# Performance work log

Measured on AMD Instinct MI355X. Metric: run time of the kernel, lower is better.

The kernel has to match this reference:

```python
import jax, jax.numpy as jnp
import numpy as np

NUM_HEADS = 16
HEAD_DIM = 64
D_MODEL = 1024
WINDOW = 256
ROPE_BASE = 10000.0
LN_EPS = 1e-5


def setup_inputs() -> dict:
    key = jax.random.key(0)
    k1, k2, k3, k4 = jax.random.split(key, 4)
    B, S, D = 1, 2048, D_MODEL
    x = jax.random.normal(k1, (B, S, D), dtype=jnp.float32)
    state = jax.random.normal(k2, (B, D), dtype=jnp.float32)
    # nn.Linear(d, 3d, bias=False): y = x @ W_qkv with W_qkv: [D, 3D]
    W_qkv = jax.random.normal(k3, (D, 3 * D), dtype=jnp.float32) / np.sqrt(D)
    W_out = jax.random.normal(k4, (D, D), dtype=jnp.float32) / np.sqrt(D)
    ln_gamma = jnp.ones((D,), dtype=jnp.float32)
    ln_beta = jnp.zeros((D,), dtype=jnp.float32)
    return {"x": x, "state": state, "W_qkv": W_qkv, "W_out": W_out,
            "ln_gamma": ln_gamma, "ln_beta": ln_beta}


def _rotate_half(t):
    h = t.shape[-1] // 2
    return jnp.concatenate([-t[..., h:], t[..., :h]], axis=-1)


def _rope(q, k):
    # q, k: [B, H, S, Hd]
    S, Hd = q.shape[2], q.shape[3]
    inv_freq = 1.0 / (ROPE_BASE ** (jnp.arange(0, Hd, 2, dtype=jnp.float32) / Hd))
    ang = jnp.arange(S, dtype=jnp.float32)[:, None] * inv_freq[None, :]  # [S, Hd/2]
    cos = jnp.concatenate([jnp.cos(ang), jnp.cos(ang)], axis=-1)[None, None]  # [1,1,S,Hd]
    sin = jnp.concatenate([jnp.sin(ang), jnp.sin(ang)], axis=-1)[None, None]
    return q * cos + _rotate_half(q) * sin, k * cos + _rotate_half(k) * sin


def _local_causal_mask(S):
    idx = jnp.arange(S)
    dist = idx[:, None] - idx[None, :]
    allowed = (dist >= 0) & (dist <= WINDOW)
    # Faithful to source: allowed positions get 1.0 (softmax-shift-invariant), else -inf
    return jnp.where(allowed, 1.0, -jnp.inf).astype(jnp.float32)[None, None]


def reference(x, state, W_qkv, W_out, ln_gamma, ln_beta):
    B, S, D = x.shape
    H, Hd = NUM_HEADS, HEAD_DIM
    qkv = (x @ W_qkv).reshape(B, S, 3, H, Hd).transpose(2, 0, 3, 1, 4)  # [3,B,H,S,Hd]
    q, k, v = qkv[0], qkv[1], qkv[2]
    q, k = _rope(q, k)
    scores = jnp.einsum("bhsd,bhtd->bhst", q, k) / np.sqrt(Hd) + _local_causal_mask(S)
    attn = jax.nn.softmax(scores, axis=-1)
    out = jnp.einsum("bhst,bhtd->bhsd", attn, v)  # [B,H,S,Hd]
    out = out.transpose(0, 2, 1, 3).reshape(B, S, D)
    res = x + out @ W_out
    mu = jnp.mean(res, axis=-1, keepdims=True)
    var = jnp.var(res, axis=-1, keepdims=True)
    y = (res - mu) * jax.lax.rsqrt(var + LN_EPS) * ln_gamma + ln_beta
    return y, state
```

## Files before the change

### kernel.cpp

```cpp
#include <hip/hip_runtime.h>
#include <math.h>

#define S_LEN 2048
#define DMODEL 1024
#define NHEADS 16
#define HDIM 64
#define WIN 256
#define N_QKV 3072

typedef __attribute__((ext_vector_type(8))) short s16x8;
typedef __attribute__((ext_vector_type(8))) _Float16 f16x8;
typedef __attribute__((ext_vector_type(4))) _Float16 f16x4;
typedef __attribute__((ext_vector_type(4))) float f32x4;

typedef __attribute__((address_space(1))) const void gas_void;
typedef __attribute__((address_space(3))) void las_void;

__device__ inline unsigned short f2bf(float f) {
    unsigned int u = __float_as_uint(f);
    u += 0x7FFFu + ((u >> 16) & 1u);
    return (unsigned short)(u >> 16);
}
__device__ inline float bf2f(unsigned short h) {
    return __uint_as_float(((unsigned int)h) << 16);
}

__global__ __launch_bounds__(256) void cvt_f16(
    const float* __restrict__ src, _Float16* __restrict__ dst)
{
    int i = blockIdx.x * 256 + threadIdx.x;
    float4 v = *(const float4*)&src[i * 4];
    f16x4 o;
    o[0] = (_Float16)v.x; o[1] = (_Float16)v.y;
    o[2] = (_Float16)v.z; o[3] = (_Float16)v.w;
    *(f16x4*)&dst[i * 4] = o;
}

__global__ __launch_bounds__(256) void rope_tab_k(float2* __restrict__ tab)
{
    int idx = blockIdx.x * 256 + threadIdx.x;
    int s = idx >> 5, i = idx & 31;
    float inv = expf(-(float)i * 0.2878231366242553f);
    float ang = (float)s * inv;
    tab[idx] = make_float2(cosf(ang), sinf(ang));
}

__global__ __launch_bounds__(256) void transpose_cvt(
    const float* __restrict__ W, _Float16* __restrict__ T, int K, int N)
{
    __shared__ float t[32][33];
    const int tx = threadIdx.x & 31;
    const int ty = threadIdx.x >> 5;
    const int n0 = blockIdx.x * 32, k0 = blockIdx.y * 32;

    #pragma unroll
    for (int i = 0; i < 4; ++i)
        t[ty + i * 8][tx] = W[(size_t)(k0 + ty + i * 8) * N + n0 + tx];
    __syncthreads();
    #pragma unroll
    for (int i = 0; i < 4; ++i) {
        int n = n0 + ty + i * 8;
        T[(size_t)n * K + k0 + tx] = (_Float16)t[tx][ty + i * 8];
    }
}

template<int BM, int BN, bool RES>
__global__ __launch_bounds__(256) void gemm_lds(
    const _Float16* __restrict__ A, const _Float16* __restrict__ B,
    const float* __restrict__ resid, float* __restrict__ C,
    int M, int N, int K)
{
    constexpr int WM = BM / 2, WN = BN / 2;
    constexpr int MI = WM / 16, NJ = WN / 16;

    __shared__ _Float16 As[BM * 32];
    __shared__ _Float16 Bs[BN * 32];

    const int tid = threadIdx.x;
    const int w = tid >> 6, lane = tid & 63;
    const int m16 = lane & 15, g = lane >> 4;
    const int wr = w >> 1, wc = w & 1;
    const int bm = blockIdx.y * BM, bn = blockIdx.x * BN;

    const int srow = lane >> 2;
    const int sgran = (lane & 3) ^ (srow & 3);

    f32x4 acc[MI][NJ];
    #pragma unroll
    for (int i = 0; i < MI; ++i)
        #pragma unroll
        for (int j = 0; j < NJ; ++j) acc[i][j] = (f32x4)(0.0f);

    for (int kt = 0; kt < K / 32; ++kt) {
        const int k0 = kt * 32;
        __syncthreads();
        #pragma unroll
        for (int p = 0; p < BM / 64; ++p) {
            int row = p * 64 + w * 16 + srow;
            __builtin_amdgcn_global_load_lds(
                (gas_void*)&A[(size_t)(bm + row) * K + k0 + sgran * 8],
                (las_void*)&As[(p * 64 + w * 16) * 32], 16, 0, 0);
        }
        #pragma unroll
        for (int p = 0; p < BN / 64; ++p) {
            int row = p * 64 + w * 16 + srow;
            __builtin_amdgcn_global_load_lds(
                (gas_void*)&B[(size_t)(bn + row) * K + k0 + sgran * 8],
                (las_void*)&Bs[(p * 64 + w * 16) * 32], 16, 0, 0);
        }
        __syncthreads();

        f16x8 af[MI], bf_[NJ];
        #pragma unroll
        for (int i = 0; i < MI; ++i) {
            int row = wr * WM + i * 16 + m16;
            af[i] = *(const f16x8*)&As[row * 32 + ((g ^ (row & 3)) << 3)];
        }
        #pragma unroll
        for (int j = 0; j < NJ; ++j) {
            int row = wc * WN + j * 16 + m16;
            bf_[j] = *(const f16x8*)&Bs[row * 32 + ((g ^ (row & 3)) << 3)];
        }
        #pragma unroll
        for (int j = 0; j < NJ; ++j)
            #pragma unroll
            for (int i = 0; i < MI; ++i)
                acc[i][j] = __builtin_amdgcn_mfma_f32_16x16x32_f16(
                    af[i], bf_[j], acc[i][j], 0, 0, 0);
    }

    const int g4 = g * 4;
    #pragma unroll
    for (int i = 0; i < MI; ++i)
        #pragma unroll
        for (int j = 0; j < NJ; ++j) {
            int col = bn + wc * WN + j * 16 + m16;
            #pragma unroll
            for (int r = 0; r < 4; ++r) {
                int row = bm + wr * WM + i * 16 + g4 + r;
                float val = acc[i][j][r];
                if (RES) val += resid[(size_t)row * N + col];
                C[(size_t)row * N + col] = val;
            }
        }
}

__global__ __launch_bounds__(256) void rope_scatter(
    const float* __restrict__ qkv, const float2* __restrict__ tab,
    _Float16* __restrict__ qf, _Float16* __restrict__ kf)
{
    int idx = blockIdx.x * 256 + threadIdx.x;
    int s  = idx >> 10;
    int r  = idx & 1023;
    int hd = r & 63;
    int h  = r >> 6;
    const float* row = qkv + (size_t)s * N_QKV;

    float qv = row[r];
    float kv = row[DMODEL + r];

    float2 cs = tab[s * 32 + (hd & 31)];
    int   pr  = (hd < 32) ? r + 32 : r - 32;
    float sgn = (hd < 32) ? -1.0f : 1.0f;

    float qo = (qv * cs.x + sgn * row[pr] * cs.y) * 0.125f;
    float ko =  kv * cs.x + sgn * row[DMODEL + pr] * cs.y;

    size_t o = ((size_t)h * S_LEN + s) * HDIM + hd;
    qf[o] = (_Float16)qo;
    kf[o] = (_Float16)ko;
}

__global__ __launch_bounds__(256) void v_transpose(
    const float* __restrict__ qkv, unsigned short* __restrict__ vT)
{
    __shared__ float t[64][65];
    const int s0 = blockIdx.x * 64;
    const int h  = blockIdx.y;
    const int tid = threadIdx.x;
    const int dq  = (tid & 15) * 4;
    const int sl0 = tid >> 4;

    #pragma unroll
    for (int p = 0; p < 4; ++p) {
        int sl = sl0 + p * 16;
        float4 v = *(const float4*)&qkv[(size_t)(s0 + sl) * N_QKV + 2 * DMODEL + h * HDIM + dq];
        t[sl][dq] = v.x; t[sl][dq + 1] = v.y; t[sl][dq + 2] = v.z; t[sl][dq + 3] = v.w;
    }
    __syncthreads();
    #pragma unroll
    for (int p = 0; p < 2; ++p) {
        int u = tid + p * 256;
        int d = u >> 3, sb = (u & 7) * 8;
        s16x8 o;
        #pragma unroll
        for (int i = 0; i < 8; ++i) o[i] = (short)f2bf(t[sb + i][d]);
        *(s16x8*)&vT[((size_t)h * HDIM + d) * S_LEN + s0 + sb] = o;
    }
}

#define KP 72
__global__ __launch_bounds__(256, 3) void attn_mfma(
    const _Float16* __restrict__ qg, const _Float16* __restrict__ kg,
    const unsigned short* __restrict__ vTg, _Float16* __restrict__ oh)
{
    __shared__ __align__(16) _Float16 Ks[64][KP];
    __shared__ __align__(16) unsigned short Vt[64][KP];
    __shared__ __align__(16) unsigned short Pw[4][16][40];

    const int h   = blockIdx.y;
    const int s0  = blockIdx.x * 64;
    const int tid = threadIdx.x;
    const int w   = tid >> 6, lane = tid & 63;
    const int m16 = lane & 15, g = lane >> 4;
    const int t_base = s0 - 256;

    const int qrow = s0 + w * 16 + m16;
    const _Float16* qp = qg + ((size_t)h * S_LEN + qrow) * HDIM;
    f16x8 qf[2];
    qf[0] = *(const f16x8*)&qp[g * 8];
    qf[1] = *(const f16x8*)&qp[32 + g * 8];

    const int qb_ = w * 16 + m16;
    int lo_b = 256 - s0; if (lo_b < qb_) lo_b = qb_;
    const int hi_b = qb_ + 256;

    f32x4 O[4];
    #pragma unroll
    for (int nt = 0; nt < 4; ++nt) O[nt] = (f32x4)(0.0f);
    float l_r[4] = {0.0f, 0.0f, 0.0f, 0.0f};
    float m_col = -1e30f;

    const int stage_min = (s0 >= 256) ? 0 : ((193 - s0 + 63) >> 6);

    for (int st = stage_min; st < 5; ++st) {
        __syncthreads();
        const int t0s = t_base + st * 64;
        #pragma unroll
        for (int pp = 0; pp < 2; ++pp) {
            int u = tid + pp * 256;
            int row = u >> 3, cb = (u & 7) * 8;
            int t = t0s + row;
            f16x8 kv = {};
            if (t >= 0)
                kv = *(const f16x8*)&kg[((size_t)h * S_LEN + t) * HDIM + cb];
            *(f16x8*)&Ks[row][cb] = kv;
        }
        #pragma unroll
        for (int pp = 0; pp < 2; ++pp) {
            int u = tid + pp * 256;
            int d = u >> 3, kb = (u & 7) * 8;
            int t = t0s + kb;
            s16x8 vv = {};
            if (t >= 0)
                vv = *(const s16x8*)&vTg[((size_t)h * HDIM + d) * S_LEN + t];
            *(s16x8*)&Vt[d][kb] = vv;
        }
        __syncthreads();

        #pragma unroll
        for (int ch = 0; ch < 2; ++ch) {
            f32x4 sc[2];
            #pragma unroll
            for (int kt2 = 0; kt2 < 2; ++kt2) {
                int krow = ch * 32 + kt2 * 16 + m16;
                f16x8 k0 = *(const f16x8*)&Ks[krow][g * 8];
                f16x8 k1 = *(const f16x8*)&Ks[krow][32 + g * 8];
                f32x4 a = (f32x4)(0.0f);
                a = __builtin_amdgcn_mfma_f32_16x16x32_f16(k0, qf[0], a, 0, 0, 0);
                a = __builtin_amdgcn_mfma_f32_16x16x32_f16(k1, qf[1], a, 0, 0, 0);
                sc[kt2] = a;
            }

            float scm[8];
            float pmax = -1e30f;
            #pragma unroll
            for (int kt2 = 0; kt2 < 2; ++kt2)
                #pragma unroll
                for (int r = 0; r < 4; ++r) {
                    int ki = st * 64 + ch * 32 + kt2 * 16 + 4 * g + r;
                    bool vd = (ki >= lo_b) && (ki <= hi_b);
                    float s_ = vd ? sc[kt2][r] : -1e30f;
                    scm[kt2 * 4 + r] = s_;
                    pmax = fmaxf(pmax, s_);
                }
            pmax = fmaxf(pmax, __shfl_xor(pmax, 16));
            pmax = fmaxf(pmax, __shfl_xor(pmax, 32));
            float mnew = fmaxf(m_col, pmax);

            float p[8];
            float psum = 0.0f;
            #pragma unroll
            for (int i = 0; i < 8; ++i) {
                float e = (scm[i] > -9e29f) ? __expf(scm[i] - mnew) : 0.0f;
                p[i] = e;
                psum += e;
            }
            psum += __shfl_xor(psum, 16);
            psum += __shfl_xor(psum, 32);
            float scale = __expf(m_col - mnew);
            m_col = mnew;

            #pragma unroll
            for (int r = 0; r < 4; ++r) {
                float sr = __shfl(scale, 4 * g + r);
                float ps = __shfl(psum, 4 * g + r);
                l_r[r] = l_r[r] * sr + ps;
                O[0][r] *= sr; O[1][r] *= sr; O[2][r] *= sr; O[3][r] *= sr;
            }

            unsigned int d0, d1, d2, d3;
            asm("v_cvt_pk_bf16_f32 %0, %1, %2" : "=v"(d0) : "v"(p[0]), "v"(p[1]));
            asm("v_cvt_pk_bf16_f32 %0, %1, %2" : "=v"(d1) : "v"(p[2]), "v"(p[3]));
            asm("v_cvt_pk_bf16_f32 %0, %1, %2" : "=v"(d2) : "v"(p[4]), "v"(p[5]));
            asm("v_cvt_pk_bf16_f32 %0, %1, %2" : "=v"(d3) : "v"(p[6]), "v"(p[7]));
            *(uint2*)&Pw[w][m16][4 * g]      = make_uint2(d0, d1);
            *(uint2*)&Pw[w][m16][16 + 4 * g] = make_uint2(d2, d3);
            asm volatile("s_waitcnt lgkmcnt(0)" ::: "memory");
            __builtin_amdgcn_sched_barrier(0);
            s16x8 pa = *(const s16x8*)&Pw[w][m16][g * 8];

            #pragma unroll
            for (int nt = 0; nt < 4; ++nt) {
                s16x8 vb = *(const s16x8*)&Vt[nt * 16 + m16][ch * 32 + g * 8];
                O[nt] = __builtin_amdgcn_mfma_f32_16x16x32_bf16(pa, vb, O[nt], 0, 0, 0);
            }
        }
    }

    #pragma unroll
    for (int r = 0; r < 4; ++r) {
        float linv = 1.0f / l_r[r];
        int srow = s0 + w * 16 + 4 * g + r;
        size_t obase = (size_t)srow * DMODEL + h * HDIM;
        #pragma unroll
        for (int nt = 0; nt < 4; ++nt)
            oh[obase + nt * 16 + m16] = (_Float16)(O[nt][r] * linv);
    }
}

__global__ __launch_bounds__(256) void layernorm_k(
    const float* __restrict__ res, const float* __restrict__ gamma,
    const float* __restrict__ beta, float* __restrict__ y)
{
    const int row  = blockIdx.x;
    const int tid  = threadIdx.x;
    const int wave = tid >> 6;
    const int lane = tid & 63;
    const float* r = res + (size_t)row * DMODEL;

    float4 xv = *(const float4*)&r[tid * 4];
    float ssum = xv.x + xv.y + xv.z + xv.w;
    float ssq  = xv.x * xv.x + xv.y * xv.y + xv.z * xv.z + xv.w * xv.w;

    #pragma unroll
    for (int off = 1; off < 64; off <<= 1) {
        ssum += __shfl_xor(ssum, off);
        ssq  += __shfl_xor(ssq, off);
    }

    __shared__ float wsum[4], wsq[4];
    if (lane == 0) { wsum[wave] = ssum; wsq[wave] = ssq; }
    __syncthreads();

    float tot  = wsum[0] + wsum[1] + wsum[2] + wsum[3];
    float tot2 = wsq[0] + wsq[1] + wsq[2] + wsq[3];
    float mu   = tot * (1.0f / DMODEL);
    float var  = tot2 * (1.0f / DMODEL) - mu * mu;
    float rstd = rsqrtf(var + 1e-5f);

    float4 gm = *(const float4*)&gamma[tid * 4];
    float4 be = *(const float4*)&beta[tid * 4];
    float4 yo;
    yo.x = (xv.x - mu) * rstd * gm.x + be.x;
    yo.y = (xv.y - mu) * rstd * gm.y + be.y;
    yo.z = (xv.z - mu) * rstd * gm.z + be.z;
    yo.w = (xv.w - mu) * rstd * gm.w + be.w;
    *(float4*)&y[(size_t)row * DMODEL + tid * 4] = yo;
}

extern "C" void kernel_launch(void* const* d_in, const int* in_sizes, int n_in,
                              void* d_out, int out_size, void* d_ws, size_t ws_size,
                              hipStream_t stream) {
    const float* x     = (const float*)d_in[0];
    const float* state = (const float*)d_in[1];
    const float* Wqkv  = (const float*)d_in[2];
    const float* Wout  = (const float*)d_in[3];
    const float* gamma = (const float*)d_in[4];
    const float* beta  = (const float*)d_in[5];
    float* out = (float*)d_out;

    char* base = (char*)d_ws;
    float*     qkv_raw = (float*)base;
    _Float16*  ah      = (_Float16*)base;
    float*     res     = (float*)(base + 8388608);
    _Float16*  qf      = (_Float16*)(base + 25165824);
    _Float16*  kf      = (_Float16*)(base + 29360128);
    unsigned short* vT = (unsigned short*)(base + 33554432);
    _Float16*  WqkvT   = (_Float16*)(base + 37748736);
    _Float16*  WoutT   = (_Float16*)(base + 44040192);
    _Float16*  xh      = (_Float16*)(base + 46137344);
    float2*    tab     = (float2*)(base + 50331648);

    cvt_f16<<<(S_LEN * DMODEL) / 1024, 256, 0, stream>>>(x, xh);
    rope_tab_k<<<(S_LEN * 32) / 256, 256, 0, stream>>>(tab);
    transpose_cvt<<<dim3(N_QKV / 32, DMODEL / 32), 256, 0, stream>>>(
        Wqkv, WqkvT, DMODEL, N_QKV);
    transpose_cvt<<<dim3(DMODEL / 32, DMODEL / 32), 256, 0, stream>>>(
        Wout, WoutT, DMODEL, DMODEL);

    gemm_lds<128, 128, false>
        <<<dim3(N_QKV / 128, S_LEN / 128), 256, 0, stream>>>(
            xh, WqkvT, nullptr, qkv_raw, S_LEN, N_QKV, DMODEL);

    rope_scatter<<<(S_LEN * DMODEL) / 256, 256, 0, stream>>>(
        qkv_raw, tab, qf, kf);

    v_transpose<<<dim3(S_LEN / 64, NHEADS), 256, 0, stream>>>(qkv_raw, vT);

    attn_mfma<<<dim3(S_LEN / 64, NHEADS), 256, 0, stream>>>(qf, kf, vT, ah);

    gemm_lds<64, 64, true>
        <<<dim3(DMODEL / 64, S_LEN / 64), 256, 0, stream>>>(
            ah, WoutT, x, res, S_LEN, DMODEL, DMODEL);

    layernorm_k<<<S_LEN, 256, 0, stream>>>(res, gamma, beta, out);

    hipMemcpyAsync(out + (size_t)S_LEN * DMODEL, state,
                   (size_t)DMODEL * sizeof(float),
                   hipMemcpyDeviceToDevice, stream);
}
```

Measured before the change: 161.6 us.

## Fuse weight transposes and QKV prep, emit f16 QKV, widen GEMM K-tile

Merges the two weight transpose launches into one, makes the QKV GEMM write f16 instead of f32, and fuses RoPE scatter and V transpose into a single prep kernel reading the f16 buffer. The GEMM K-tile doubles from 32 to 64 with an 8-way XOR swizzle, which halves the number of barrier pairs per tile. The attention kernel raises wave priority around its MFMA blocks. Together these cut launch count and intermediate memory traffic. The cost is that the pre-RoPE QKV values are rounded to f16 before rotation, and the GEMMs need more LDS.

```diff
diff --git a/kernel.cpp b/kernel.cpp
--- a/kernel.cpp
+++ b/kernel.cpp
@@ -45,13 +45,19 @@
     tab[idx] = make_float2(cosf(ang), sinf(ang));
 }
 
-__global__ __launch_bounds__(256) void transpose_cvt(
-    const float* __restrict__ W, _Float16* __restrict__ T, int K, int N)
+__global__ __launch_bounds__(256) void transpose_cvt2(
+    const float* __restrict__ W1, const float* __restrict__ W2,
+    _Float16* __restrict__ T1, _Float16* __restrict__ T2)
 {
     __shared__ float t[32][33];
+    const float* W;
+    _Float16* T;
+    int N, n0;
+    if (blockIdx.x < 96) { W = W1; T = T1; N = N_QKV; n0 = blockIdx.x * 32; }
+    else                 { W = W2; T = T2; N = DMODEL; n0 = (blockIdx.x - 96) * 32; }
+    const int K = DMODEL, k0 = blockIdx.y * 32;
     const int tx = threadIdx.x & 31;
     const int ty = threadIdx.x >> 5;
-    const int n0 = blockIdx.x * 32, k0 = blockIdx.y * 32;
 
     #pragma unroll
     for (int i = 0; i < 4; ++i)
@@ -64,17 +70,18 @@
     }
 }
 
-template<int BM, int BN, bool RES>
+template<int BM, int BN, bool RES, bool F16OUT>
 __global__ __launch_bounds__(256) void gemm_lds(
     const _Float16* __restrict__ A, const _Float16* __restrict__ B,
-    const float* __restrict__ resid, float* __restrict__ C,
+    const float* __restrict__ resid, void* __restrict__ Cout,
     int M, int N, int K)
 {
     constexpr int WM = BM / 2, WN = BN / 2;
     constexpr int MI = WM / 16, NJ = WN / 16;
-
-    __shared__ _Float16 As[BM * 32];
-    __shared__ _Float16 Bs[BN * 32];
+    constexpr int PA = BM * 8 / 256, PB = BN * 8 / 256;
+
+    __shared__ _Float16 As[BM * 64];
+    __shared__ _Float16 Bs[BN * 64];
 
     const int tid = threadIdx.x;
     const int w = tid >> 6, lane = tid & 63;
@@ -82,8 +89,7 @@
     const int wr = w >> 1, wc = w & 1;
     const int bm = blockIdx.y * BM, bn = blockIdx.x * BN;
 
-    const int srow = lane >> 2;
-    const int sgran = (lane & 3) ^ (srow & 3);
+    const int sgran = (lane & 7) ^ (lane >> 3);
 
     f32x4 acc[MI][NJ];
     #pragma unroll
@@ -91,42 +97,45 @@
         #pragma unroll
         for (int j = 0; j < NJ; ++j) acc[i][j] = (f32x4)(0.0f);
 
-    for (int kt = 0; kt < K / 32; ++kt) {
-        const int k0 = kt * 32;
+    for (int kt = 0; kt < K / 64; ++kt) {
+        const int k0 = kt * 64;
         __syncthreads();
         #pragma unroll
-        for (int p = 0; p < BM / 64; ++p) {
-            int row = p * 64 + w * 16 + srow;
+        for (int p = 0; p < PA; ++p) {
+            int row = (p * 256 + tid) >> 3;
             __builtin_amdgcn_global_load_lds(
                 (gas_void*)&A[(size_t)(bm + row) * K + k0 + sgran * 8],
-                (las_void*)&As[(p * 64 + w * 16) * 32], 16, 0, 0);
-        }
-        #pragma unroll
-        for (int p = 0; p < BN / 64; ++p) {
-            int row = p * 64 + w * 16 + srow;
+                (las_void*)&As[(p * 256 + w * 64) * 8], 16, 0, 0);
+        }
+        #pragma unroll
+        for (int p = 0; p < PB; ++p) {
+            int row = (p * 256 + tid) >> 3;
             __builtin_amdgcn_global_load_lds(
                 (gas_void*)&B[(size_t)(bn + row) * K + k0 + sgran * 8],
-                (las_void*)&Bs[(p * 64 + w * 16) * 32], 16, 0, 0);
+                (las_void*)&Bs[(p * 256 + w * 64) * 8], 16, 0, 0);
         }
         __syncthreads();
 
-        f16x8 af[MI], bf_[NJ];
-        #pragma unroll
-        for (int i = 0; i < MI; ++i) {
-            int row = wr * WM + i * 16 + m16;
-            af[i] = *(const f16x8*)&As[row * 32 + ((g ^ (row & 3)) << 3)];
-        }
-        #pragma unroll
-        for (int j = 0; j < NJ; ++j) {
-            int row = wc * WN + j * 16 + m16;
-            bf_[j] = *(const f16x8*)&Bs[row * 32 + ((g ^ (row & 3)) << 3)];
-        }
-        #pragma unroll
-        for (int j = 0; j < NJ; ++j)
-            #pragma unroll
-            for (int i = 0; i < MI; ++i)
-                acc[i][j] = __builtin_amdgcn_mfma_f32_16x16x32_f16(
-                    af[i], bf_[j], acc[i][j], 0, 0, 0);
+        #pragma unroll
+        for (int kh = 0; kh < 2; ++kh) {
+            f16x8 af[MI], bf_[NJ];
+            #pragma unroll
+            for (int i = 0; i < MI; ++i) {
+                int row = wr * WM + i * 16 + m16;
+                af[i] = *(const f16x8*)&As[row * 64 + (((kh * 4 + g) ^ (row & 7)) << 3)];
+            }
+            #pragma unroll
+            for (int j = 0; j < NJ; ++j) {
+                int row = wc * WN + j * 16 + m16;
+                bf_[j] = *(const f16x8*)&Bs[row * 64 + (((kh * 4 + g) ^ (row & 7)) << 3)];
+            }
+            #pragma unroll
+            for (int j = 0; j < NJ; ++j)
+                #pragma unroll
+                for (int i = 0; i < MI; ++i)
+                    acc[i][j] = __builtin_amdgcn_mfma_f32_16x16x32_f16(
+                        af[i], bf_[j], acc[i][j], 0, 0, 0);
+        }
     }
 
     const int g4 = g * 4;
@@ -139,62 +148,66 @@
             for (int r = 0; r < 4; ++r) {
                 int row = bm + wr * WM + i * 16 + g4 + r;
                 float val = acc[i][j][r];
-                if (RES) val += resid[(size_t)row * N + col];
-                C[(size_t)row * N + col] = val;
-            }
-        }
-}
-
-__global__ __launch_bounds__(256) void rope_scatter(
-    const float* __restrict__ qkv, const float2* __restrict__ tab,
-    _Float16* __restrict__ qf, _Float16* __restrict__ kf)
-{
-    int idx = blockIdx.x * 256 + threadIdx.x;
-    int s  = idx >> 10;
-    int r  = idx & 1023;
-    int hd = r & 63;
-    int h  = r >> 6;
-    const float* row = qkv + (size_t)s * N_QKV;
-
-    float qv = row[r];
-    float kv = row[DMODEL + r];
-
-    float2 cs = tab[s * 32 + (hd & 31)];
-    int   pr  = (hd < 32) ? r + 32 : r - 32;
-    float sgn = (hd < 32) ? -1.0f : 1.0f;
-
-    float qo = (qv * cs.x + sgn * row[pr] * cs.y) * 0.125f;
-    float ko =  kv * cs.x + sgn * row[DMODEL + pr] * cs.y;
-
-    size_t o = ((size_t)h * S_LEN + s) * HDIM + hd;
-    qf[o] = (_Float16)qo;
-    kf[o] = (_Float16)ko;
-}
-
-__global__ __launch_bounds__(256) void v_transpose(
-    const float* __restrict__ qkv, unsigned short* __restrict__ vT)
-{
-    __shared__ float t[64][65];
+                if constexpr (F16OUT) {
+                    ((_Float16*)Cout)[(size_t)row * N + col] = (_Float16)val;
+                } else {
+                    if (RES) val += resid[(size_t)row * N + col];
+                    ((float*)Cout)[(size_t)row * N + col] = val;
+                }
+            }
+        }
+}
+
+__global__ __launch_bounds__(256) void prep_qkv(
+    const _Float16* __restrict__ qkv, const float2* __restrict__ tab,
+    _Float16* __restrict__ qf, _Float16* __restrict__ kf,
+    unsigned short* __restrict__ vT)
+{
+    __shared__ _Float16 vt[64][72];
     const int s0 = blockIdx.x * 64;
     const int h  = blockIdx.y;
     const int tid = threadIdx.x;
-    const int dq  = (tid & 15) * 4;
-    const int sl0 = tid >> 4;
-
-    #pragma unroll
-    for (int p = 0; p < 4; ++p) {
-        int sl = sl0 + p * 16;
-        float4 v = *(const float4*)&qkv[(size_t)(s0 + sl) * N_QKV + 2 * DMODEL + h * HDIM + dq];
-        t[sl][dq] = v.x; t[sl][dq + 1] = v.y; t[sl][dq + 2] = v.z; t[sl][dq + 3] = v.w;
+
+    #pragma unroll
+    for (int p = 0; p < 2; ++p) {
+        int u = p * 256 + tid;
+        int sl = u >> 3;
+        int d0 = (u & 7) * 8;
+        int s = s0 + sl;
+        const _Float16* rowp = qkv + (size_t)s * N_QKV;
+
+        f16x8 qv = *(const f16x8*)&rowp[h * 64 + d0];
+        f16x8 kv = *(const f16x8*)&rowp[DMODEL + h * 64 + d0];
+        int pd = (d0 < 32) ? d0 + 32 : d0 - 32;
+        f16x8 qp_ = *(const f16x8*)&rowp[h * 64 + pd];
+        f16x8 kp_ = *(const f16x8*)&rowp[DMODEL + h * 64 + pd];
+        float sgn = (d0 < 32) ? -1.0f : 1.0f;
+
+        f16x8 qo, ko;
+        #pragma unroll
+        for (int j = 0; j < 8; ++j) {
+            float2 cs = tab[s * 32 + ((d0 + j) & 31)];
+            float qr = (float)qv[j] * cs.x + sgn * (float)qp_[j] * cs.y;
+            float kr = (float)kv[j] * cs.x + sgn * (float)kp_[j] * cs.y;
+            qo[j] = (_Float16)(qr * 0.125f);
+            ko[j] = (_Float16)kr;
+        }
+        size_t o = ((size_t)h * S_LEN + s) * HDIM + d0;
+        *(f16x8*)&qf[o] = qo;
+        *(f16x8*)&kf[o] = ko;
+
+        f16x8 vv = *(const f16x8*)&rowp[2 * DMODEL + h * 64 + d0];
+        #pragma unroll
+        for (int j = 0; j < 8; ++j) vt[sl][d0 + j] = vv[j];
     }
     __syncthreads();
     #pragma unroll
     for (int p = 0; p < 2; ++p) {
-        int u = tid + p * 256;
+        int u = p * 256 + tid;
         int d = u >> 3, sb = (u & 7) * 8;
         s16x8 o;
         #pragma unroll
-        for (int i = 0; i < 8; ++i) o[i] = (short)f2bf(t[sb + i][d]);
+        for (int i = 0; i < 8; ++i) o[i] = (short)f2bf((float)vt[sb + i][d]);
         *(s16x8*)&vT[((size_t)h * HDIM + d) * S_LEN + s0 + sb] = o;
     }
 }
@@ -261,6 +274,7 @@
         #pragma unroll
         for (int ch = 0; ch < 2; ++ch) {
             f32x4 sc[2];
+            __builtin_amdgcn_s_setprio(1);
             #pragma unroll
             for (int kt2 = 0; kt2 < 2; ++kt2) {
                 int krow = ch * 32 + kt2 * 16 + m16;
@@ -271,6 +285,7 @@
                 a = __builtin_amdgcn_mfma_f32_16x16x32_f16(k1, qf[1], a, 0, 0, 0);
                 sc[kt2] = a;
             }
+            __builtin_amdgcn_s_setprio(0);
 
             float scm[8];
             float pmax = -1e30f;
@@ -320,11 +335,13 @@
             __builtin_amdgcn_sched_barrier(0);
             s16x8 pa = *(const s16x8*)&Pw[w][m16][g * 8];
 
+            __builtin_amdgcn_s_setprio(1);
             #pragma unroll
             for (int nt = 0; nt < 4; ++nt) {
                 s16x8 vb = *(const s16x8*)&Vt[nt * 16 + m16][ch * 32 + g * 8];
                 O[nt] = __builtin_amdgcn_mfma_f32_16x16x32_bf16(pa, vb, O[nt], 0, 0, 0);
             }
+            __builtin_amdgcn_s_setprio(0);
         }
     }
 
@@ -391,36 +408,31 @@
     float* out = (float*)d_out;
 
     char* base = (char*)d_ws;
-    float*     qkv_raw = (float*)base;
-    _Float16*  ah      = (_Float16*)base;
-    float*     res     = (float*)(base + 8388608);
-    _Float16*  qf      = (_Float16*)(base + 25165824);
-    _Float16*  kf      = (_Float16*)(base + 29360128);
-    unsigned short* vT = (unsigned short*)(base + 33554432);
-    _Float16*  WqkvT   = (_Float16*)(base + 37748736);
-    _Float16*  WoutT   = (_Float16*)(base + 44040192);
-    _Float16*  xh      = (_Float16*)(base + 46137344);
-    float2*    tab     = (float2*)(base + 50331648);
+    _Float16*  qkv16 = (_Float16*)base;
+    _Float16*  ah    = (_Float16*)base;
+    float*     res   = (float*)(base + 4194304);
+    _Float16*  qf    = (_Float16*)(base + 16777216);
+    _Float16*  kf    = (_Float16*)(base + 20971520);
+    unsigned short* vT = (unsigned short*)(base + 25165824);
+    _Float16*  WqkvT = (_Float16*)(base + 29360128);
+    _Float16*  WoutT = (_Float16*)(base + 35651584);
+    _Float16*  xh    = (_Float16*)(base + 37748736);
+    float2*    tab   = (float2*)(base + 41943040);
 
     cvt_f16<<<(S_LEN * DMODEL) / 1024, 256, 0, stream>>>(x, xh);
     rope_tab_k<<<(S_LEN * 32) / 256, 256, 0, stream>>>(tab);
-    transpose_cvt<<<dim3(N_QKV / 32, DMODEL / 32), 256, 0, stream>>>(
-        Wqkv, WqkvT, DMODEL, N_QKV);
-    transpose_cvt<<<dim3(DMODEL / 32, DMODEL / 32), 256, 0, stream>>>(
-        Wout, WoutT, DMODEL, DMODEL);
-
-    gemm_lds<128, 128, false>
+    transpose_cvt2<<<dim3(128, 32), 256, 0, stream>>>(Wqkv, Wout, WqkvT, WoutT);
+
+    gemm_lds<128, 128, false, true>
         <<<dim3(N_QKV / 128, S_LEN / 128), 256, 0, stream>>>(
-            xh, WqkvT, nullptr, qkv_raw, S_LEN, N_QKV, DMODEL);
-
-    rope_scatter<<<(S_LEN * DMODEL) / 256, 256, 0, stream>>>(
-        qkv_raw, tab, qf, kf);
-
-    v_transpose<<<dim3(S_LEN / 64, NHEADS), 256, 0, stream>>>(qkv_raw, vT);
+            xh, WqkvT, nullptr, qkv16, S_LEN, N_QKV, DMODEL);
+
+    prep_qkv<<<dim3(S_LEN / 64, NHEADS), 256, 0, stream>>>(
+        qkv16, tab, qf, kf, vT);
 
     attn_mfma<<<dim3(S_LEN / 64, NHEADS), 256, 0, stream>>>(qf, kf, vT, ah);
 
-    gemm_lds<64, 64, true>
+    gemm_lds<64, 64, true, false>
         <<<dim3(DMODEL / 64, S_LEN / 64), 256, 0, stream>>>(
             ah, WoutT, x, res, S_LEN, DMODEL, DMODEL);
 
```

After: 149.1 us. 1.08x faster.
